# Optimization experiments

Hardware: AMD Instinct MI355X
Metric: run time of the kernel (lower is better)

The kernel has to match this reference:

```python
import jax, jax.numpy as jnp
import numpy as np

N_UP, N_DOWN, M, D, K, F, L, B = 16, 16, 4, 128, 64, 32, 3, 1024
N = N_UP + N_DOWN
H_W = 45  # round(sqrt(F*K)), hidden dim of the 2-layer w MLP
LOG2 = float(np.log(2.0))


def ssp(x):
    # shifted softplus activation used by deepqmc
    return jax.nn.softplus(x) - LOG2


def _pair_blocks(n_up, n_down):
    # replicate idx_perm(N,2) grouped by i, then idx_pair_spin partition
    n = n_up + n_down
    i = np.repeat(np.arange(n), n - 1)
    j = np.concatenate([np.concatenate([np.arange(k), np.arange(k + 1, n)]) for k in range(n)])
    blocks = []
    for mi, mj, ri, rj in [(True, True, n_up, max(n_up - 1, 0)),
                           (True, False, n_up, n_down),
                           (False, True, n_down, n_up),
                           (False, False, n_down, max(n_down - 1, 0))]:
        mask = ((i < n_up) == mi) & ((j < n_up) == mj)
        blocks.append((i[mask].reshape(ri, rj), j[mask].reshape(ri, rj)))
    return blocks

_BLOCKS = _pair_blocks(N_UP, N_DOWN)
_CHANS = [0, 1, 1, 0]  # same, anti, anti, same (w/g channel index; 2 = nuclear)


def setup_inputs() -> dict:
    key = jax.random.key(0)
    ks = jax.random.split(key, 12)
    s = 0.1
    return {
        'edges_elec': jax.random.normal(ks[0], (B, N, N, F), jnp.float32),
        'edges_nuc': jax.random.normal(ks[1], (B, N, M, F), jnp.float32),
        'X': jax.random.normal(ks[2], (1, D), jnp.float32) * s,
        'Y': jax.random.normal(ks[3], (M, K), jnp.float32) * s,
        'wW1': jax.random.normal(ks[4], (L, 3, H_W, F), jnp.float32) * s,
        'wb1': jax.random.normal(ks[5], (L, 3, H_W), jnp.float32) * s,
        'wW2': jax.random.normal(ks[6], (L, 3, K, H_W), jnp.float32) * s,
        'wb2': jax.random.normal(ks[7], (L, 3, K), jnp.float32) * s,
        'hW': jax.random.normal(ks[8], (L, K, D), jnp.float32) * s,
        'hb': jax.random.normal(ks[9], (L, K), jnp.float32) * s,
        'gW': jax.random.normal(ks[10], (L, 3, D, K), jnp.float32) * s,
        'gb': jax.random.normal(ks[11], (L, 3, D), jnp.float32) * s,
    }


def reference(edges_elec, edges_nuc, X, Y, wW1, wb1, wW2, wb2, hW, hb, gW, gb):
    def w_mlp(l, c, e):
        # 2-layer log-dim MLP: F -> H_W -> K with SSP in between
        return ssp(e @ wW1[l, c].T + wb1[l, c]) @ wW2[l, c].T + wb2[l, c]

    b = edges_nuc.shape[0]
    x = jnp.broadcast_to(X, (b, N, D))  # initial electron embeddings (n_up==n_down)
    for l in range(L):
        h = x @ hW[l].T + hb[l]  # shared h subnet: [b,N,K]
        zs = []
        for (ii, jj), c in zip(_BLOCKS, _CHANS):
            e = edges_elec[:, ii, jj, :]               # [b, ri, rj, F] gather
            msg = w_mlp(l, c, e) * h[:, jj, :]          # [b, ri, rj, K]
            zs.append(msg.sum(axis=-2))                 # segment-sum over j
        z_same = jnp.concatenate([zs[0], zs[3]], axis=-2)  # up then down
        z_anti = jnp.concatenate([zs[1], zs[2]], axis=-2)
        z_nuc = jnp.einsum('bnmk,mk->bnk', w_mlp(l, 2, edges_nuc), Y)
        update = (z_same @ gW[l, 0].T + gb[l, 0]
                  + z_anti @ gW[l, 1].T + gb[l, 1]
                  + z_nuc @ gW[l, 2].T + gb[l, 2])
        x = x + update  # resnet
    return x
```

## Files before the change

### kernel.cpp

```cpp
#include <hip/hip_runtime.h>
#include <math.h>

#define N_   32
#define NUP_ 16
#define M_   4
#define D_   128
#define K_   64
#define F_   32
#define H_   45
#define L_   3
#define LOG2_ 0.69314718055994530942f

typedef __attribute__((ext_vector_type(8))) short short8;
typedef __attribute__((ext_vector_type(4))) float float4v;

__device__ __forceinline__ float ssp(float v) {
    return __logf(fmaf(0.5f, __expf(v), 0.5f));
}

__device__ __forceinline__ unsigned short f2bf(float x) {
    unsigned int u = __float_as_uint(x);
    return (unsigned short)((u + 0x7FFFu + ((u >> 16) & 1u)) >> 16);
}

__device__ __forceinline__ unsigned int cvtpk(float x, float y) {
    unsigned int r;
    asm("v_cvt_pk_bf16_f32 %0, %1, %2" : "=v"(r) : "v"(x), "v"(y));
    return r;
}

__global__ __launch_bounds__(256) void prep_kernel(
    const float* __restrict__ wW1, const float* __restrict__ wb2_unused,
    const float* __restrict__ wW2, const float* __restrict__ wb2,
    const float* __restrict__ gW,  const float* __restrict__ hW,
    const float* __restrict__ gb,
    short* __restrict__ w1B, short* __restrict__ w2B,
    short* __restrict__ gB,  short* __restrict__ hB, float* __restrict__ gbs)
{
    int blk = blockIdx.x;
    int t = threadIdx.x;
    if (blk < 27) {
        int lc = blk / 3, nt = blk % 3;
        short* dst = w1B + (size_t)blk * 512;
        for (int idx = t; idx < 512; idx += 256) {
            int lane = idx >> 3, jj = idx & 7;
            int k = ((lane >> 4) << 3) + jj;
            int n = nt * 16 + (lane & 15);
            float v = (n < H_) ? wW1[((size_t)lc * H_ + n) * F_ + k] : 0.0f;
            dst[idx] = (short)f2bf(v);
        }
    } else if (blk < 99) {
        int b3 = blk - 27;
        int lc = b3 >> 3, rem = b3 & 7, ks = rem >> 2, nt = rem & 3;
        short* dst = w2B + (size_t)b3 * 512;
        for (int idx = t; idx < 512; idx += 256) {
            int lane = idx >> 3, jj = idx & 7;
            int p = ks * 32 + ((lane >> 4) << 3) + jj;
            int n = nt * 16 + (lane & 15);
            float v;
            if (p == 3) v = wb2[(size_t)lc * K_ + n];
            else if ((p & 3) < 3) {
                int u = (p & 3) * 16 + (p >> 2);
                v = (u < H_) ? wW2[((size_t)lc * K_ + n) * H_ + u] : 0.0f;
            } else v = 0.0f;
            dst[idx] = (short)f2bf(v);
        }
    } else if (blk < 243) {
        int g = blk - 99;
        int l = g / 48, rem = g % 48;
        short* dst = gB + (size_t)g * 512;
        for (int idx = t; idx < 512; idx += 256) {
            int lane = idx >> 3, jj = idx & 7;
            int k = (rem >> 3) * 32 + ((lane >> 4) << 3) + jj;
            int c = k >> 6, kk = k & 63;
            int n = ((rem & 7) * 16) + (lane & 15);
            dst[idx] = (short)f2bf(gW[(((size_t)l * 3 + c) * D_ + n) * K_ + kk]);
        }
    } else if (blk < 275) {
        int hh = blk - 243;
        int li = hh >> 4, rem = hh & 15;
        short* dst = hB + (size_t)hh * 512;
        for (int idx = t; idx < 512; idx += 256) {
            int lane = idx >> 3, jj = idx & 7;
            int p = (rem >> 2) * 32 + ((lane >> 4) << 3) + jj;
            int d = (p & 7) * 16 + (p >> 3);
            int n = ((rem & 3) * 16) + (lane & 15);
            dst[idx] = (short)f2bf(hW[(((size_t)(li + 1)) * K_ + n) * D_ + d]);
        }
    } else {
        for (int idx = t; idx < 384; idx += 256) {
            int l = idx >> 7, d = idx & 127;
            gbs[idx] = gb[((size_t)l * 3 + 0) * D_ + d]
                     + gb[((size_t)l * 3 + 1) * D_ + d]
                     + gb[((size_t)l * 3 + 2) * D_ + d];
        }
    }
}

__global__ __launch_bounds__(64) void h0_kernel(
    const float* __restrict__ X, const float* __restrict__ hW,
    const float* __restrict__ hb, float* __restrict__ h0)
{
    int k = threadIdx.x;
    float a = hb[k];
    const float* w = hW + (size_t)k * D_;
    #pragma unroll 8
    for (int dd = 0; dd < D_; ++dd) a += w[dd] * X[dd];
    h0[k] = a;
}

#define WSTRIDE 68
#define HDS 72
__global__ __launch_bounds__(256, 8) void edge_kernel(
    const float* __restrict__ ee, const float* __restrict__ en,
    const float* __restrict__ Y,
    const short* __restrict__ w1B, const float* __restrict__ wb1,
    const short* __restrict__ w2B,
    const float* __restrict__ h, const float* __restrict__ h0,
    unsigned short* __restrict__ zb, int l, int hmode)
{
    __shared__ float wrow[36 * WSTRIDE];
    __shared__ short hd_s[4][16 * HDS];

    const int tid  = threadIdx.x;
    const int wv   = tid >> 6;
    const int lane = tid & 63;
    const int quad = lane >> 4;
    const int l16  = lane & 15;
    const int b    = blockIdx.x >> 3;
    const int i    = ((blockIdx.x & 7) << 2) + wv;
    const int bi   = (b << 5) + i;

    {
        int row = tid >> 3;
        int col = (tid & 7) * 8;
        const float* src = hmode ? (h + ((size_t)(b * N_ + row)) * K_ + col) : (h0 + col);
        float4 v0 = *(const float4*)(src);
        float4 v1 = *(const float4*)(src + 4);
        *(float4*)(wrow + row * WSTRIDE + col)     = v0;
        *(float4*)(wrow + row * WSTRIDE + col + 4) = v1;
        if (tid < 32) {
            int r2 = tid >> 3, o2 = (tid & 7) * 8;
            float4 y0 = *(const float4*)(Y + (size_t)r2 * K_ + o2);
            float4 y1 = *(const float4*)(Y + (size_t)r2 * K_ + o2 + 4);
            *(float4*)(wrow + (32 + r2) * WSTRIDE + o2)     = y0;
            *(float4*)(wrow + (32 + r2) * WSTRIDE + o2 + 4) = y1;
        }
    }
    __syncthreads();

    const int cA = (i < NUP_) ? 0 : 1;
    short* hd = hd_s[wv];
    const float c3  = (l16 == 0) ? 1.0f : 0.0f;
    const int   ri  = i & 3;
    const int   tqi = (i & 15) >> 2;
    const int   tti = i >> 4;

    #pragma unroll
    for (int t = 0; t < 2; ++t) {
        const int c  = (t == 0) ? cA : 1 - cA;
        const int lc = l * 3 + c;

        const float* ep = ee + (((size_t)bi * N_) + t * 16 + l16) * F_ + quad * 8;
        float4 fa = *(const float4*)(ep);
        float4 fb = *(const float4*)(ep + 4);
        union { short8 s; unsigned int u[4]; } A;
        A.u[0] = cvtpk(fa.x, fa.y); A.u[1] = cvtpk(fa.z, fa.w);
        A.u[2] = cvtpk(fb.x, fb.y); A.u[3] = cvtpk(fb.z, fb.w);

        float4v acc1[3];
        #pragma unroll
        for (int nt = 0; nt < 3; ++nt) {
            int col = nt * 16 + l16;
            float b1c = (col < H_) ? wb1[(size_t)lc * H_ + col] : 0.0f;
            acc1[nt] = (float4v){b1c, b1c, b1c, b1c};
            short8 bf = *(const short8*)(w1B + (((size_t)lc * 3 + nt) << 9) + (lane << 3));
            acc1[nt] = __builtin_amdgcn_mfma_f32_16x16x32_bf16(A.s, bf, acc1[nt], 0, 0, 0);
        }

        const bool deadq = (tti == t) && (quad == tqi);
        #pragma unroll
        for (int r = 0; r < 4; ++r) {
            float s0 = ssp(acc1[0][r]);
            float s1 = ssp(acc1[1][r]);
            float s2 = ssp(acc1[2][r]);
            uint2 pr;
            pr.x = cvtpk(s0, s1);
            pr.y = cvtpk(s2, c3);
            if (deadq && (r == ri)) { pr.x = 0u; pr.y = 0u; }
            *(uint2*)(hd + (quad * 4 + r) * HDS + 4 * l16) = pr;
        }

        float4v acc2[4];
        #pragma unroll
        for (int nt = 0; nt < 4; ++nt) acc2[nt] = (float4v){0.f, 0.f, 0.f, 0.f};
        #pragma unroll
        for (int ks = 0; ks < 2; ++ks) {
            short8 a2 = *(const short8*)(hd + l16 * HDS + ks * 32 + quad * 8);
            #pragma unroll
            for (int nt = 0; nt < 4; ++nt) {
                short8 bf = *(const short8*)(w2B + ((((size_t)lc * 2 + ks) * 4 + nt) << 9) + (lane << 3));
                acc2[nt] = __builtin_amdgcn_mfma_f32_16x16x32_bf16(a2, bf, acc2[nt], 0, 0, 0);
            }
        }

        float p0 = 0.f, p1 = 0.f, p2 = 0.f, p3 = 0.f;
        #pragma unroll
        for (int r = 0; r < 4; ++r) {
            const int jrow = t * 16 + quad * 4 + r;
            const float* wr = wrow + jrow * WSTRIDE + l16;
            p0 += acc2[0][r] * wr[0];
            p1 += acc2[1][r] * wr[16];
            p2 += acc2[2][r] * wr[32];
            p3 += acc2[3][r] * wr[48];
        }

        const bool qlo = (quad & 1) != 0;
        const bool qhi = (quad & 2) != 0;
        float u  = qlo ? p1 : p0;
        float us = qlo ? p0 : p1;
        u += __shfl_xor(us, 16);
        float w  = qlo ? p3 : p2;
        float ws = qlo ? p2 : p3;
        w += __shfl_xor(ws, 16);
        float v  = qhi ? w : u;
        float vs = qhi ? u : w;
        v += __shfl_xor(vs, 32);

        zb[(size_t)bi * 192 + c * 64 + lane] = (unsigned short)cvtpk(v, v);
    }

    if (wv == 0) {
        const int lc = l * 3 + 2;

        const float* np = en + ((size_t)bi * M_ + l16) * F_ + quad * 8;
        float4 fa = *(const float4*)(np);
        float4 fb = *(const float4*)(np + 4);
        union { short8 s; unsigned int u[4]; } A;
        A.u[0] = cvtpk(fa.x, fa.y); A.u[1] = cvtpk(fa.z, fa.w);
        A.u[2] = cvtpk(fb.x, fb.y); A.u[3] = cvtpk(fb.z, fb.w);

        float4v acc1[3];
        #pragma unroll
        for (int nt = 0; nt < 3; ++nt) {
            int col = nt * 16 + l16;
            float b1c = (col < H_) ? wb1[(size_t)lc * H_ + col] : 0.0f;
            acc1[nt] = (float4v){b1c, b1c, b1c, b1c};
            short8 bf = *(const short8*)(w1B + (((size_t)lc * 3 + nt) << 9) + (lane << 3));
            acc1[nt] = __builtin_amdgcn_mfma_f32_16x16x32_bf16(A.s, bf, acc1[nt], 0, 0, 0);
        }

        #pragma unroll
        for (int r = 0; r < 4; ++r) {
            float s0 = ssp(acc1[0][r]);
            float s1 = ssp(acc1[1][r]);
            float s2 = ssp(acc1[2][r]);
            uint2 pr;
            pr.x = cvtpk(s0, s1);
            pr.y = cvtpk(s2, c3);
            *(uint2*)(hd + (quad * 4 + r) * HDS + 4 * l16) = pr;
        }

        float4v acc2[4];
        #pragma unroll
        for (int nt = 0; nt < 4; ++nt) acc2[nt] = (float4v){0.f, 0.f, 0.f, 0.f};
        #pragma unroll
        for (int ks = 0; ks < 2; ++ks) {
            short8 a2 = *(const short8*)(hd + l16 * HDS + ks * 32 + quad * 8);
            #pragma unroll
            for (int nt = 0; nt < 4; ++nt) {
                short8 bf = *(const short8*)(w2B + ((((size_t)lc * 2 + ks) * 4 + nt) << 9) + (lane << 3));
                acc2[nt] = __builtin_amdgcn_mfma_f32_16x16x32_bf16(a2, bf, acc2[nt], 0, 0, 0);
            }
        }

        float p0 = 0.f, p1 = 0.f, p2 = 0.f, p3 = 0.f;
        #pragma unroll
        for (int r = 0; r < 4; ++r) {
            const float* wr = wrow + (32 + r) * WSTRIDE + l16;
            p0 += acc2[0][r] * wr[0];
            p1 += acc2[1][r] * wr[16];
            p2 += acc2[2][r] * wr[32];
            p3 += acc2[3][r] * wr[48];
        }
        unsigned short* zo = zb + (size_t)(bi + quad) * 192 + 128 + l16;
        zo[0]  = (unsigned short)cvtpk(p0, p0);
        zo[16] = (unsigned short)cvtpk(p1, p1);
        zo[32] = (unsigned short)cvtpk(p2, p2);
        zo[48] = (unsigned short)cvtpk(p3, p3);
    }
}

#define HXS 136
__global__ __launch_bounds__(256) void fuse_kernel(
    const unsigned short* __restrict__ zb, const short* __restrict__ gB,
    const float* __restrict__ gbs, const float* __restrict__ X,
    const short* __restrict__ hB, const float* __restrict__ hb,
    float* __restrict__ xout, float* __restrict__ hout,
    int l, int first, int compute_h)
{
    __shared__ short hx_s[2][16 * HXS];

    const int tid  = threadIdx.x;
    const int wv   = tid >> 6;
    const int lane = tid & 63;
    const int quad = lane >> 4;
    const int l16  = lane & 15;
    const int pair = wv >> 1;
    const int half = wv & 1;
    const int nt0  = half * 4;
    const int bi0  = (blockIdx.x * 2 + pair) * 16;

    float4v ax[4];
    #pragma unroll
    for (int nt = 0; nt < 4; ++nt) ax[nt] = (float4v){0.f, 0.f, 0.f, 0.f};
    const short* gb_ = gB + (size_t)l * 48 * 512;
    const short* zrow = (const short*)zb + ((size_t)(bi0 + l16)) * 192;
    #pragma unroll
    for (int ks = 0; ks < 6; ++ks) {
        short8 az = *(const short8*)(zrow + ks * 32 + quad * 8);
        #pragma unroll
        for (int nt = 0; nt < 4; ++nt) {
            short8 bf = *(const short8*)(gb_ + (((size_t)ks * 8 + nt0 + nt) << 9) + (lane << 3));
            ax[nt] = __builtin_amdgcn_mfma_f32_16x16x32_bf16(az, bf, ax[nt], 0, 0, 0);
        }
    }

    float gv[4], xb[4];
    #pragma unroll
    for (int nt = 0; nt < 4; ++nt) {
        gv[nt] = gbs[(size_t)l * D_ + (nt0 + nt) * 16 + l16];
        if (first) xb[nt] = X[(nt0 + nt) * 16 + l16];
    }
    short* hx = hx_s[pair];
    #pragma unroll
    for (int r = 0; r < 4; ++r) {
        int row = quad * 4 + r;
        size_t gi = ((size_t)(bi0 + row)) * D_ + l16;
        float xv[4];
        #pragma unroll
        for (int nt = 0; nt < 4; ++nt) {
            float xo = (first ? xb[nt] : xout[gi + (nt0 + nt) * 16]) + gv[nt] + ax[nt][r];
            xout[gi + (nt0 + nt) * 16] = xo;
            xv[nt] = xo;
        }
        if (compute_h) {
            uint2 P;
            P.x = cvtpk(xv[0], xv[1]);
            P.y = cvtpk(xv[2], xv[3]);
            *(uint2*)(hx + row * HXS + 8 * l16 + 4 * half) = P;
        }
    }
    if (!compute_h) return;
    __syncthreads();

    float4v ah[2];
    #pragma unroll
    for (int nt = 0; nt < 2; ++nt) ah[nt] = (float4v){0.f, 0.f, 0.f, 0.f};
    const short* hb_ = hB + (size_t)l * 16 * 512;
    #pragma unroll
    for (int ks = 0; ks < 4; ++ks) {
        short8 a = *(const short8*)(hx + l16 * HXS + ks * 32 + quad * 8);
        #pragma unroll
        for (int nt = 0; nt < 2; ++nt) {
            short8 bf = *(const short8*)(hb_ + (((size_t)ks * 4 + half * 2 + nt) << 9) + (lane << 3));
            ah[nt] = __builtin_amdgcn_mfma_f32_16x16x32_bf16(a, bf, ah[nt], 0, 0, 0);
        }
    }
    float hbv[2];
    #pragma unroll
    for (int nt = 0; nt < 2; ++nt) hbv[nt] = hb[((size_t)(l + 1)) * K_ + (half * 2 + nt) * 16 + l16];
    #pragma unroll
    for (int nt = 0; nt < 2; ++nt)
        #pragma unroll
        for (int r = 0; r < 4; ++r)
            hout[((size_t)(bi0 + quad * 4 + r)) * K_ + (half * 2 + nt) * 16 + l16] = ah[nt][r] + hbv[nt];
}

extern "C" void kernel_launch(void* const* d_in, const int* in_sizes, int n_in,
                              void* d_out, int out_size, void* d_ws, size_t ws_size,
                              hipStream_t stream)
{
    const float* ee  = (const float*)d_in[0];
    const float* en  = (const float*)d_in[1];
    const float* X   = (const float*)d_in[2];
    const float* Y   = (const float*)d_in[3];
    const float* wW1 = (const float*)d_in[4];
    const float* wb1 = (const float*)d_in[5];
    const float* wW2 = (const float*)d_in[6];
    const float* wb2 = (const float*)d_in[7];
    const float* hW  = (const float*)d_in[8];
    const float* hb  = (const float*)d_in[9];
    const float* gW  = (const float*)d_in[10];
    const float* gb  = (const float*)d_in[11];
    float* xout = (float*)d_out;

    char* ws = (char*)d_ws;
    float*          h   = (float*)(ws);
    unsigned short* zb  = (unsigned short*)(ws + 8388608);
    float*          h0  = (float*)(ws + 8388608 + 12582912);
    short*          w1B = (short*)(ws + 20971520 + 256);
    short*          w2B = w1B + (size_t)27 * 512;
    short*          gB  = w2B + (size_t)72 * 512;
    short*          hB  = gB  + (size_t)144 * 512;
    float*          gbs = (float*)(hB + (size_t)32 * 512);

    prep_kernel<<<276, 256, 0, stream>>>(wW1, wb1, wW2, wb2, gW, hW, gb,
                                         w1B, w2B, gB, hB, gbs);
    h0_kernel<<<1, 64, 0, stream>>>(X, hW, hb, h0);

    edge_kernel<<<8192, 256, 0, stream>>>(ee, en, Y, w1B, wb1, w2B, h, h0, zb, 0, 0);
    fuse_kernel<<<1024, 256, 0, stream>>>(zb, gB, gbs, X, hB, hb, xout, h, 0, 1, 1);
    edge_kernel<<<8192, 256, 0, stream>>>(ee, en, Y, w1B, wb1, w2B, h, h0, zb, 1, 1);
    fuse_kernel<<<1024, 256, 0, stream>>>(zb, gB, gbs, X, hB, hb, xout, h, 1, 0, 1);
    edge_kernel<<<8192, 256, 0, stream>>>(ee, en, Y, w1B, wb1, w2B, h, h0, zb, 2, 1);
    fuse_kernel<<<1024, 256, 0, stream>>>(zb, gB, gbs, X, hB, hb, xout, h, 2, 0, 0);
}
```

Baseline: 400.4 us.

## Compute first MLP layer transposed so its output feeds second MFMA from registers

The first-layer MFMA now has its operands swapped, giving a transposed result whose per-lane layout matches the A-operand layout the second-layer MFMA expects. The w2 weight packing is permuted to match, and the bias and self-pair masking move to register-level constants. This removes the per-wave LDS staging buffer and its write/read round trip between the two layers, which lowers LDS use and synchronisation. It relies on a careful index permutation in the prep kernel, where a mistake would silently corrupt the results.

After: 420.0 us. 1.05x slower.

```diff
diff --git a/kernel.cpp b/kernel.cpp
--- a/kernel.cpp
+++ b/kernel.cpp
@@ -30,7 +30,7 @@
 }
 
 __global__ __launch_bounds__(256) void prep_kernel(
-    const float* __restrict__ wW1, const float* __restrict__ wb2_unused,
+    const float* __restrict__ wW1, const float* __restrict__ wb1_unused,
     const float* __restrict__ wW2, const float* __restrict__ wb2,
     const float* __restrict__ gW,  const float* __restrict__ hW,
     const float* __restrict__ gb,
@@ -57,11 +57,16 @@
             int lane = idx >> 3, jj = idx & 7;
             int p = ks * 32 + ((lane >> 4) << 3) + jj;
             int n = nt * 16 + (lane & 15);
+            int q = (p & 31) >> 3, j = p & 7;
             float v;
-            if (p == 3) v = wb2[(size_t)lc * K_ + n];
-            else if ((p & 3) < 3) {
-                int u = (p & 3) * 16 + (p >> 2);
+            if (p < 32) {
+                int u = (j >> 2) * 16 + q * 4 + (j & 3);
+                v = wW2[((size_t)lc * K_ + n) * H_ + u];
+            } else if (j < 4) {
+                int u = 32 + q * 4 + j;
                 v = (u < H_) ? wW2[((size_t)lc * K_ + n) * H_ + u] : 0.0f;
+            } else if (p == 36) {
+                v = wb2[(size_t)lc * K_ + n];
             } else v = 0.0f;
             dst[idx] = (short)f2bf(v);
         }
@@ -110,7 +115,6 @@
 }
 
 #define WSTRIDE 68
-#define HDS 72
 __global__ __launch_bounds__(256, 8) void edge_kernel(
     const float* __restrict__ ee, const float* __restrict__ en,
     const float* __restrict__ Y,
@@ -120,7 +124,6 @@
     unsigned short* __restrict__ zb, int l, int hmode)
 {
     __shared__ float wrow[36 * WSTRIDE];
-    __shared__ short hd_s[4][16 * HDS];
 
     const int tid  = threadIdx.x;
     const int wv   = tid >> 6;
@@ -149,59 +152,66 @@
     }
     __syncthreads();
 
-    const int cA = (i < NUP_) ? 0 : 1;
-    short* hd = hd_s[wv];
-    const float c3  = (l16 == 0) ? 1.0f : 0.0f;
-    const int   ri  = i & 3;
-    const int   tqi = (i & 15) >> 2;
-    const int   tti = i >> 4;
+    const int cA  = (i < NUP_) ? 0 : 1;
+    const int tti = i >> 4;
+    const int sil = i & 15;
+    const int hq  = quad * 4;
+    const unsigned int biasu = (quad == 0) ? 0x00003F80u : 0u;
 
     #pragma unroll
     for (int t = 0; t < 2; ++t) {
         const int c  = (t == 0) ? cA : 1 - cA;
         const int lc = l * 3 + c;
+        const float* wlc = wb1 + (size_t)lc * H_;
 
         const float* ep = ee + (((size_t)bi * N_) + t * 16 + l16) * F_ + quad * 8;
         float4 fa = *(const float4*)(ep);
         float4 fb = *(const float4*)(ep + 4);
-        union { short8 s; unsigned int u[4]; } A;
-        A.u[0] = cvtpk(fa.x, fa.y); A.u[1] = cvtpk(fa.z, fa.w);
-        A.u[2] = cvtpk(fb.x, fb.y); A.u[3] = cvtpk(fb.z, fb.w);
-
+        union { short8 s; unsigned int u[4]; } E;
+        E.u[0] = cvtpk(fa.x, fa.y); E.u[1] = cvtpk(fa.z, fa.w);
+        E.u[2] = cvtpk(fb.x, fb.y); E.u[3] = cvtpk(fb.z, fb.w);
+
+        const bool g3 = (hq < 12);
         float4v acc1[3];
+        acc1[0] = (float4v){wlc[hq], wlc[hq + 1], wlc[hq + 2], wlc[hq + 3]};
+        acc1[1] = (float4v){wlc[16 + hq], wlc[17 + hq], wlc[18 + hq], wlc[19 + hq]};
+        {
+            float b1 = wlc[g3 ? (33 + hq) : 0];
+            float b2 = wlc[g3 ? (34 + hq) : 0];
+            float b3 = wlc[g3 ? (35 + hq) : 0];
+            acc1[2] = (float4v){wlc[32 + hq], g3 ? b1 : 0.0f, g3 ? b2 : 0.0f, g3 ? b3 : 0.0f};
+        }
+
         #pragma unroll
         for (int nt = 0; nt < 3; ++nt) {
-            int col = nt * 16 + l16;
-            float b1c = (col < H_) ? wb1[(size_t)lc * H_ + col] : 0.0f;
-            acc1[nt] = (float4v){b1c, b1c, b1c, b1c};
-            short8 bf = *(const short8*)(w1B + (((size_t)lc * 3 + nt) << 9) + (lane << 3));
-            acc1[nt] = __builtin_amdgcn_mfma_f32_16x16x32_bf16(A.s, bf, acc1[nt], 0, 0, 0);
-        }
-
-        const bool deadq = (tti == t) && (quad == tqi);
-        #pragma unroll
-        for (int r = 0; r < 4; ++r) {
-            float s0 = ssp(acc1[0][r]);
-            float s1 = ssp(acc1[1][r]);
-            float s2 = ssp(acc1[2][r]);
-            uint2 pr;
-            pr.x = cvtpk(s0, s1);
-            pr.y = cvtpk(s2, c3);
-            if (deadq && (r == ri)) { pr.x = 0u; pr.y = 0u; }
-            *(uint2*)(hd + (quad * 4 + r) * HDS + 4 * l16) = pr;
+            short8 wf = *(const short8*)(w1B + (((size_t)lc * 3 + nt) << 9) + (lane << 3));
+            acc1[nt] = __builtin_amdgcn_mfma_f32_16x16x32_bf16(wf, E.s, acc1[nt], 0, 0, 0);
+        }
+
+        union { short8 s; unsigned int u[4]; } A0, A1;
+        A0.u[0] = cvtpk(ssp(acc1[0][0]), ssp(acc1[0][1]));
+        A0.u[1] = cvtpk(ssp(acc1[0][2]), ssp(acc1[0][3]));
+        A0.u[2] = cvtpk(ssp(acc1[1][0]), ssp(acc1[1][1]));
+        A0.u[3] = cvtpk(ssp(acc1[1][2]), ssp(acc1[1][3]));
+        A1.u[0] = cvtpk(ssp(acc1[2][0]), ssp(acc1[2][1]));
+        A1.u[1] = cvtpk(ssp(acc1[2][2]), ssp(acc1[2][3]));
+        A1.u[2] = biasu;
+        A1.u[3] = 0u;
+        const bool deadl = (t == tti) && (l16 == sil);
+        if (deadl) {
+            A0.u[0] = 0u; A0.u[1] = 0u; A0.u[2] = 0u; A0.u[3] = 0u;
+            A1.u[0] = 0u; A1.u[1] = 0u; A1.u[2] = 0u;
         }
 
         float4v acc2[4];
         #pragma unroll
         for (int nt = 0; nt < 4; ++nt) acc2[nt] = (float4v){0.f, 0.f, 0.f, 0.f};
         #pragma unroll
-        for (int ks = 0; ks < 2; ++ks) {
-            short8 a2 = *(const short8*)(hd + l16 * HDS + ks * 32 + quad * 8);
-            #pragma unroll
-            for (int nt = 0; nt < 4; ++nt) {
-                short8 bf = *(const short8*)(w2B + ((((size_t)lc * 2 + ks) * 4 + nt) << 9) + (lane << 3));
-                acc2[nt] = __builtin_amdgcn_mfma_f32_16x16x32_bf16(a2, bf, acc2[nt], 0, 0, 0);
-            }
+        for (int nt = 0; nt < 4; ++nt) {
+            short8 bf0 = *(const short8*)(w2B + ((((size_t)lc * 2 + 0) * 4 + nt) << 9) + (lane << 3));
+            acc2[nt] = __builtin_amdgcn_mfma_f32_16x16x32_bf16(A0.s, bf0, acc2[nt], 0, 0, 0);
+            short8 bf1 = *(const short8*)(w2B + ((((size_t)lc * 2 + 1) * 4 + nt) << 9) + (lane << 3));
+            acc2[nt] = __builtin_amdgcn_mfma_f32_16x16x32_bf16(A1.s, bf1, acc2[nt], 0, 0, 0);
         }
 
         float p0 = 0.f, p1 = 0.f, p2 = 0.f, p3 = 0.f;
@@ -232,46 +242,50 @@
 
     if (wv == 0) {
         const int lc = l * 3 + 2;
+        const float* wlc = wb1 + (size_t)lc * H_;
 
         const float* np = en + ((size_t)bi * M_ + l16) * F_ + quad * 8;
         float4 fa = *(const float4*)(np);
         float4 fb = *(const float4*)(np + 4);
-        union { short8 s; unsigned int u[4]; } A;
-        A.u[0] = cvtpk(fa.x, fa.y); A.u[1] = cvtpk(fa.z, fa.w);
-        A.u[2] = cvtpk(fb.x, fb.y); A.u[3] = cvtpk(fb.z, fb.w);
-
+        union { short8 s; unsigned int u[4]; } E;
+        E.u[0] = cvtpk(fa.x, fa.y); E.u[1] = cvtpk(fa.z, fa.w);
+        E.u[2] = cvtpk(fb.x, fb.y); E.u[3] = cvtpk(fb.z, fb.w);
+
+        const bool g3 = (hq < 12);
         float4v acc1[3];
+        acc1[0] = (float4v){wlc[hq], wlc[hq + 1], wlc[hq + 2], wlc[hq + 3]};
+        acc1[1] = (float4v){wlc[16 + hq], wlc[17 + hq], wlc[18 + hq], wlc[19 + hq]};
+        {
+            float b1 = wlc[g3 ? (33 + hq) : 0];
+            float b2 = wlc[g3 ? (34 + hq) : 0];
+            float b3 = wlc[g3 ? (35 + hq) : 0];
+            acc1[2] = (float4v){wlc[32 + hq], g3 ? b1 : 0.0f, g3 ? b2 : 0.0f, g3 ? b3 : 0.0f};
+        }
         #pragma unroll
         for (int nt = 0; nt < 3; ++nt) {
-            int col = nt * 16 + l16;
-            float b1c = (col < H_) ? wb1[(size_t)lc * H_ + col] : 0.0f;
-            acc1[nt] = (float4v){b1c, b1c, b1c, b1c};
-            short8 bf = *(const short8*)(w1B + (((size_t)lc * 3 + nt) << 9) + (lane << 3));
-            acc1[nt] = __builtin_amdgcn_mfma_f32_16x16x32_bf16(A.s, bf, acc1[nt], 0, 0, 0);
-        }
-
-        #pragma unroll
-        for (int r = 0; r < 4; ++r) {
-            float s0 = ssp(acc1[0][r]);
-            float s1 = ssp(acc1[1][r]);
-            float s2 = ssp(acc1[2][r]);
-            uint2 pr;
-            pr.x = cvtpk(s0, s1);
-            pr.y = cvtpk(s2, c3);
-            *(uint2*)(hd + (quad * 4 + r) * HDS + 4 * l16) = pr;
-        }
+            short8 wf = *(const short8*)(w1B + (((size_t)lc * 3 + nt) << 9) + (lane << 3));
+            acc1[nt] = __builtin_amdgcn_mfma_f32_16x16x32_bf16(wf, E.s, acc1[nt], 0, 0, 0);
+        }
+
+        union { short8 s; unsigned int u[4]; } A0, A1;
+        A0.u[0] = cvtpk(ssp(acc1[0][0]), ssp(acc1[0][1]));
+        A0.u[1] = cvtpk(ssp(acc1[0][2]), ssp(acc1[0][3]));
+        A0.u[2] = cvtpk(ssp(acc1[1][0]), ssp(acc1[1][1]));
+        A0.u[3] = cvtpk(ssp(acc1[1][2]), ssp(acc1[1][3]));
+        A1.u[0] = cvtpk(ssp(acc1[2][0]), ssp(acc1[2][1]));
+        A1.u[1] = cvtpk(ssp(acc1[2][2]), ssp(acc1[2][3]));
+        A1.u[2] = biasu;
+        A1.u[3] = 0u;
 
         float4v acc2[4];
         #pragma unroll
         for (int nt = 0; nt < 4; ++nt) acc2[nt] = (float4v){0.f, 0.f, 0.f, 0.f};
         #pragma unroll
-        for (int ks = 0; ks < 2; ++ks) {
-            short8 a2 = *(const short8*)(hd + l16 * HDS + ks * 32 + quad * 8);
-            #pragma unroll
-            for (int nt = 0; nt < 4; ++nt) {
-                short8 bf = *(const short8*)(w2B + ((((size_t)lc * 2 + ks) * 4 + nt) << 9) + (lane << 3));
-                acc2[nt] = __builtin_amdgcn_mfma_f32_16x16x32_bf16(a2, bf, acc2[nt], 0, 0, 0);
-            }
+        for (int nt = 0; nt < 4; ++nt) {
+            short8 bf0 = *(const short8*)(w2B + ((((size_t)lc * 2 + 0) * 4 + nt) << 9) + (lane << 3));
+            acc2[nt] = __builtin_amdgcn_mfma_f32_16x16x32_bf16(A0.s, bf0, acc2[nt], 0, 0, 0);
+            short8 bf1 = *(const short8*)(w2B + ((((size_t)lc * 2 + 1) * 4 + nt) << 9) + (lane << 3));
+            acc2[nt] = __builtin_amdgcn_mfma_f32_16x16x32_bf16(A1.s, bf1, acc2[nt], 0, 0, 0);
         }
 
         float p0 = 0.f, p1 = 0.f, p2 = 0.f, p3 = 0.f;
```
